# Kernel tuning notes

Hardware: AMD Instinct MI355X
Metric: run time of the kernel (lower is better)

## Reference

```python
import jax, jax.numpy as jnp
import numpy as np

DIM = 512
HIDDEN = int(DIM * 0.2)  # 102
K_TOKENS = 64
N_TOKENS = 65536
LN_EPS = 1e-5


def setup_inputs() -> dict:
    key = jax.random.key(0)
    ks = jax.random.split(key, 8)
    x = jax.random.normal(ks[0], (N_TOKENS, DIM), dtype=jnp.float32)
    ln_gamma = jnp.ones((DIM,), dtype=jnp.float32)
    ln_beta = jnp.zeros((DIM,), dtype=jnp.float32)
    W1 = jax.random.normal(ks[1], (DIM, HIDDEN), dtype=jnp.float32) / np.sqrt(DIM)
    b1 = jnp.zeros((HIDDEN,), dtype=jnp.float32)
    W2 = jax.random.normal(ks[2], (HIDDEN, K_TOKENS), dtype=jnp.float32) / np.sqrt(HIDDEN)
    b2 = jnp.zeros((K_TOKENS,), dtype=jnp.float32)
    scale = jnp.ones((1, 1), dtype=jnp.float32)
    return {
        "x": x,
        "ln_gamma": ln_gamma,
        "ln_beta": ln_beta,
        "W1": W1,
        "b1": b1,
        "W2": W2,
        "b2": b2,
        "scale": scale,
        "keeped_tokens": K_TOKENS,
    }


def reference(x, ln_gamma, ln_beta, W1, b1, W2, b2, scale, keeped_tokens):
    # LayerNorm over last dim
    mu = jnp.mean(x, axis=-1, keepdims=True)
    var = jnp.mean(jnp.square(x - mu), axis=-1, keepdims=True)
    h = (x - mu) * jax.lax.rsqrt(var + LN_EPS) * ln_gamma + ln_beta
    # fc1 + exact GELU (torch default) + dynamic fc2 scorer
    h = jax.nn.gelu(h @ W1 + b1, approximate=False)  # [N, HIDDEN]
    w = h @ W2 + b2                                   # [N, K]
    # transpose, scale, softmax over tokens
    w = w.T * scale                                   # [K, N]
    w = jax.nn.softmax(w, axis=1)
    # weighted token aggregation
    return w @ x                                      # [K, DIM]
```

## Files before the change

### kernel.cpp

```cpp
#include <hip/hip_runtime.h>
#include <math.h>

#define N_TOK 65536
#define DIM   512
#define HID   102
#define KTOK  64
#define NTILE 4096
#define LN_EPS 1e-5f

typedef __attribute__((ext_vector_type(8))) short short8;
typedef __attribute__((ext_vector_type(4))) float f32x4;

#define WS_LOGITS 0u
#define WS_PART   4194304u
#define WS_PM     (WS_PART + 4194304u)
#define WS_PS     (WS_PM + 262144u)
#define WS_W1F    (WS_PS + 262144u)
#define WS_W2F    (WS_W1F + 32768u)
#define WS_UB     (WS_W2F + 4096u)
#define WS_VV     (WS_UB + 128u)
#define WS_SMAX   (WS_VV + 128u)
#define WS_SINV   (WS_SMAX + 64u)

__device__ __forceinline__ unsigned short f2bf(float f) {
    unsigned int u = __float_as_uint(f);
    unsigned int r = (u + 0x7fffu + ((u >> 16) & 1u)) >> 16;
    return (unsigned short)r;
}
__device__ __forceinline__ float bf2f(unsigned short h) {
    return __uint_as_float(((unsigned int)h) << 16);
}

__device__ __forceinline__ void gload_lds16(const void* g, void* l) {
    __builtin_amdgcn_global_load_lds(
        (const __attribute__((address_space(1))) unsigned int*)g,
        (__attribute__((address_space(3))) unsigned int*)l, 16, 0, 0);
}

__device__ __forceinline__ void bar_lds() {
    asm volatile("s_waitcnt lgkmcnt(0)" ::: "memory");
    __builtin_amdgcn_s_barrier();
    __builtin_amdgcn_sched_barrier(0);
}

__global__ __launch_bounds__(256) void prep_k(const float* __restrict__ W1,
                                              const float* __restrict__ gamma,
                                              const float* __restrict__ W2,
                                              unsigned short* __restrict__ W1f,
                                              unsigned short* __restrict__ W2f) {
    const int idx = blockIdx.x * 256 + threadIdx.x;
    {
        const int e = idx & 7, lane = (idx >> 3) & 63;
        const int jj = (idx >> 9) & 7, kc = (idx >> 12) & 15;
        const int j = jj * 16 + (lane & 15);
        const int d = kc * 32 + (lane >> 4) * 8 + e;
        W1f[idx] = (j < HID) ? f2bf(gamma[d] * W1[d * HID + j]) : (unsigned short)0;
    }
    if (idx < 8192) {
        const int e = idx & 7, lane = (idx >> 3) & 63;
        const int kc = (idx >> 9) & 3, N = (idx >> 11) & 3;
        const int j = kc * 32 + (lane >> 4) * 8 + e;
        const int k = N * 16 + (lane & 15);
        W2f[idx] = (j < HID) ? f2bf(W2[j * KTOK + k]) : (unsigned short)0;
    }
}

__global__ __launch_bounds__(512) void prep2_k(const float* __restrict__ W1,
                                               const float* __restrict__ b1,
                                               const float* __restrict__ gamma,
                                               const float* __restrict__ beta,
                                               float* __restrict__ ub,
                                               float* __restrict__ vv) {
    __shared__ float su[4][128], sv[4][128];
    const int t = threadIdx.x;
    const int j = t & 127, q = t >> 7;
    float u = 0.0f, v = 0.0f;
    if (j < HID) {
        #pragma unroll 8
        for (int d = q * 128; d < q * 128 + 128; ++d) {
            const float wv = W1[d * HID + j];
            u = fmaf(beta[d], wv, u);
            v = fmaf(gamma[d], wv, v);
        }
    }
    su[q][j] = u; sv[q][j] = v;
    __syncthreads();
    if (q == 0) {
        ub[j] = su[0][j] + su[1][j] + su[2][j] + su[3][j] +
                ((j < HID) ? b1[j] : 0.0f);
        vv[j] = sv[0][j] + sv[1][j] + sv[2][j] + sv[3][j];
    }
}

__global__ __launch_bounds__(512) void scorer_k(const float* __restrict__ x,
                                                const unsigned short* __restrict__ W1f,
                                                const unsigned short* __restrict__ W2f,
                                                const float* __restrict__ ub,
                                                const float* __restrict__ vv,
                                                const float* __restrict__ b2,
                                                const float* __restrict__ scale,
                                                float* __restrict__ logits,
                                                float* __restrict__ pm,
                                                float* __restrict__ psum) {
    __shared__ char smem[4 * 8192];
    const int tid = threadIdx.x;
    const int lane = tid & 63;
    const int w = tid >> 6;
    const int l15 = lane & 15;
    const int hi = lane >> 4;
    const int tile = blockIdx.x * 8 + w;
    const int wt0 = tile * 16;
    char* hb = smem + w * 4096;

    gload_lds16(W1f + w * 512 + lane * 8, smem + w * 1024);
    gload_lds16(W1f + 4096 + w * 512 + lane * 8, smem + 8192 + w * 1024);

    const float* xrow = x + (size_t)(wt0 + l15) * DIM + hi * 8;
    float s = 0.0f, ss = 0.0f;
    #pragma unroll
    for (int kc = 0; kc < 16; ++kc) {
        const f32x4 a = *(const f32x4*)(xrow + kc * 32);
        const f32x4 b = *(const f32x4*)(xrow + kc * 32 + 4);
        s += a.x + a.y + a.z + a.w + b.x + b.y + b.z + b.w;
        ss += a.x * a.x + a.y * a.y + a.z * a.z + a.w * a.w +
              b.x * b.x + b.y * b.y + b.z * b.z + b.w * b.w;
        if ((kc & 7) == 7) __builtin_amdgcn_sched_barrier(0);
    }
    s += __shfl_xor(s, 16); ss += __shfl_xor(ss, 16);
    s += __shfl_xor(s, 32); ss += __shfl_xor(ss, 32);
    const float mu = s * (1.0f / 512.0f);
    const float inv = rsqrtf(ss * (1.0f / 512.0f) - mu * mu + LN_EPS);

    asm volatile("" : "+v"(xrow));

    f32x4 acc[8] = {};
    f32x4 xa = *(const f32x4*)(xrow);
    f32x4 xb = *(const f32x4*)(xrow + 4);
    #pragma unroll
    for (int kc = 0; kc < 16; ++kc) {
        f32x4 xa_n, xb_n;
        if (kc < 15) {
            xa_n = *(const f32x4*)(xrow + (kc + 1) * 32);
            xb_n = *(const f32x4*)(xrow + (kc + 1) * 32 + 4);
        }
        if (kc < 14) {
            gload_lds16(W1f + (kc + 2) * 4096 + w * 512 + lane * 8,
                        smem + ((kc + 2) & 3) * 8192 + w * 1024);
        }
        if (kc == 0 || kc == 14)
            asm volatile("s_waitcnt vmcnt(3)" ::: "memory");
        else if (kc < 14)
            asm volatile("s_waitcnt vmcnt(4)" ::: "memory");
        else
            asm volatile("s_waitcnt vmcnt(0)" ::: "memory");
        __builtin_amdgcn_sched_barrier(0);
        __builtin_amdgcn_s_barrier();
        short8 af;
        af[0] = (short)f2bf(xa.x); af[1] = (short)f2bf(xa.y);
        af[2] = (short)f2bf(xa.z); af[3] = (short)f2bf(xa.w);
        af[4] = (short)f2bf(xb.x); af[5] = (short)f2bf(xb.y);
        af[6] = (short)f2bf(xb.z); af[7] = (short)f2bf(xb.w);
        const char* bb = smem + (kc & 3) * 8192 + lane * 16;
        __builtin_amdgcn_s_setprio(1);
        #pragma unroll
        for (int jj = 0; jj < 8; ++jj) {
            const short8 bf = *(const short8*)(bb + jj * 1024);
            acc[jj] = __builtin_amdgcn_mfma_f32_16x16x32_bf16(af, bf, acc[jj], 0, 0, 0);
        }
        __builtin_amdgcn_s_setprio(0);
        xa = xa_n; xb = xb_n;
    }
    __syncthreads();

    float invr[4], muir[4];
    #pragma unroll
    for (int r = 0; r < 4; ++r) {
        const int tk = 4 * hi + r;
        const float m_ = __shfl(mu, tk);
        const float i_ = __shfl(inv, tk);
        invr[r] = i_;
        muir[r] = m_ * i_;
    }
    #pragma unroll
    for (int jj = 0; jj < 8; ++jj) {
        const int col = jj * 16 + l15;
        const float ubj = ub[col];
        const float vvj = vv[col];
        #pragma unroll
        for (int reg = 0; reg < 4; ++reg) {
            const int t = 4 * hi + reg;
            const float pre = fmaf(invr[reg], acc[jj][reg],
                                   fmaf(-muir[reg], vvj, ubj));
            const float g = 0.5f * pre * (1.0f + erff(pre * 0.70710678118f));
            *(unsigned short*)(hb + t * 256 + ((col * 2) ^ ((t & 7) << 4))) = f2bf(g);
        }
    }
    asm volatile("s_waitcnt lgkmcnt(0)" ::: "memory");
    __builtin_amdgcn_sched_barrier(0);

    f32x4 acc2[4] = {};
    {
        const unsigned short* w2 = W2f + lane * 8;
        #pragma unroll
        for (int kc = 0; kc < 4; ++kc) {
            const short8 a2 = *(const short8*)(hb + l15 * 256 +
                                               ((kc * 64 + hi * 16) ^ ((l15 & 7) << 4)));
            __builtin_amdgcn_s_setprio(1);
            #pragma unroll
            for (int nt = 0; nt < 4; ++nt) {
                const short8 bfr = *(const short8*)(w2 + (size_t)(nt * 4 + kc) * 512);
                acc2[nt] = __builtin_amdgcn_mfma_f32_16x16x32_bf16(a2, bfr, acc2[nt], 0, 0, 0);
            }
            __builtin_amdgcn_s_setprio(0);
        }
    }

    const float sc = scale[0];
    #pragma unroll
    for (int nt = 0; nt < 4; ++nt) {
        const int k = nt * 16 + l15;
        const float bb = b2[k];
        f32x4 lv;
        lv.x = (acc2[nt][0] + bb) * sc;
        lv.y = (acc2[nt][1] + bb) * sc;
        lv.z = (acc2[nt][2] + bb) * sc;
        lv.w = (acc2[nt][3] + bb) * sc;
        *(f32x4*)(logits + (size_t)k * N_TOK + wt0 + hi * 4) = lv;
        float m4 = fmaxf(fmaxf(lv.x, lv.y), fmaxf(lv.z, lv.w));
        float s4 = __expf(lv.x - m4) + __expf(lv.y - m4) +
                   __expf(lv.z - m4) + __expf(lv.w - m4);
        #pragma unroll
        for (int o = 16; o <= 32; o <<= 1) {
            const float om = __shfl_xor(m4, o);
            const float os = __shfl_xor(s4, o);
            const float nm = fmaxf(m4, om);
            s4 = s4 * __expf(m4 - nm) + os * __expf(om - nm);
            m4 = nm;
        }
        if (hi == 0) {
            pm[tile * 64 + k] = m4;
            psum[tile * 64 + k] = s4;
        }
    }
}

__global__ __launch_bounds__(256) void stats_k(const float* __restrict__ pm,
                                               const float* __restrict__ psum,
                                               float* __restrict__ smax,
                                               float* __restrict__ sinv) {
    const int k = blockIdx.x;
    const int tid = threadIdx.x;
    __shared__ float rm[4], rs[4];
    float m = -1e30f, s = 0.0f;
    for (int b = tid; b < NTILE; b += 256) {
        const float pmv = pm[b * 64 + k];
        const float psv = psum[b * 64 + k];
        const float nm = fmaxf(m, pmv);
        s = s * __expf(m - nm) + psv * __expf(pmv - nm);
        m = nm;
    }
    #pragma unroll
    for (int o = 32; o >= 1; o >>= 1) {
        const float om = __shfl_xor(m, o);
        const float os = __shfl_xor(s, o);
        const float nm = fmaxf(m, om);
        s = s * __expf(m - nm) + os * __expf(om - nm);
        m = nm;
    }
    if ((tid & 63) == 0) { rm[tid >> 6] = m; rs[tid >> 6] = s; }
    __syncthreads();
    if (tid == 0) {
        float fm = rm[0], fs = rs[0];
        for (int i = 1; i < 4; ++i) {
            const float nm = fmaxf(fm, rm[i]);
            fs = fs * __expf(fm - nm) + rs[i] * __expf(rm[i] - nm);
            fm = nm;
        }
        smax[k] = fm;
        sinv[k] = 1.0f / fs;
    }
}

__global__ __launch_bounds__(512) void agg_k(const float* __restrict__ x,
                                             const float* __restrict__ logits,
                                             const float* __restrict__ smax,
                                             const float* __restrict__ sinv,
                                             float* __restrict__ part) {
    __shared__ char fsm[40960];
    const int tid = threadIdx.x;
    const int lane = tid & 63;
    const int w = tid >> 6;
    const int l15 = lane & 15;
    const int hi = lane >> 4;
    const int dg = blockIdx.y;
    const int tb = blockIdx.x;

    const int sk = tid >> 3;
    const int snp = (tid & 7) * 8;
    const int xd = tid & 127;
    const int xnb = (tid >> 7) * 16;
    const float mk = smax[sk];
    const float ik = sinv[sk];
    const float* lrow = logits + (size_t)sk * N_TOK + tb * 512 + snp;
    const float* xcol = x + (size_t)(tb * 512 + xnb) * DIM + dg * 128 + xd;

    char* pw = fsm + (((sk >> 4) * 2 + (snp >> 5)) * 64 +
                      (sk & 15) + 16 * ((snp & 31) >> 3)) * 16;
    const int xoff0 = (((xd >> 4) * 2 + (xnb >> 5)) * 64 +
                       (xd & 15) + 16 * (((xnb & 31) >> 3) + 0)) * 16;
    const int xoff1 = (((xd >> 4) * 2 + (xnb >> 5)) * 64 +
                       (xd & 15) + 16 * (((xnb & 31) >> 3) + 1)) * 16;

    const int kt = w & 3;
    const int dgr = w >> 2;

    f32x4 acc[4] = {};

    f32x4 pa = *(const f32x4*)(lrow);
    f32x4 pb = *(const f32x4*)(lrow + 4);
    float xl[16];
    #pragma unroll
    for (int i = 0; i < 16; ++i) xl[i] = xcol[(size_t)i * DIM];

    for (int c = 0; c < 8; ++c) {
        {
            short8 pv;
            pv[0] = (short)f2bf(__expf(pa.x - mk) * ik);
            pv[1] = (short)f2bf(__expf(pa.y - mk) * ik);
            pv[2] = (short)f2bf(__expf(pa.z - mk) * ik);
            pv[3] = (short)f2bf(__expf(pa.w - mk) * ik);
            pv[4] = (short)f2bf(__expf(pb.x - mk) * ik);
            pv[5] = (short)f2bf(__expf(pb.y - mk) * ik);
            pv[6] = (short)f2bf(__expf(pb.z - mk) * ik);
            pv[7] = (short)f2bf(__expf(pb.w - mk) * ik);
            *(short8*)pw = pv;
        }
        {
            short8 h0, l0, h1, l1;
            #pragma unroll
            for (int e = 0; e < 8; ++e) {
                const float v = xl[e];
                const unsigned short hb16 = f2bf(v);
                h0[e] = (short)hb16;
                l0[e] = (short)f2bf(v - bf2f(hb16));
            }
            #pragma unroll
            for (int e = 0; e < 8; ++e) {
                const float v = xl[8 + e];
                const unsigned short hb16 = f2bf(v);
                h1[e] = (short)hb16;
                l1[e] = (short)f2bf(v - bf2f(hb16));
            }
            *(short8*)(fsm + 8192 + xoff0) = h0;
            *(short8*)(fsm + 24576 + xoff0) = l0;
            *(short8*)(fsm + 8192 + xoff1) = h1;
            *(short8*)(fsm + 24576 + xoff1) = l1;
        }
        f32x4 pa_n, pb_n;
        float xln[16];
        if (c < 7) {
            pa_n = *(const f32x4*)(lrow + (c + 1) * 64);
            pb_n = *(const f32x4*)(lrow + (c + 1) * 64 + 4);
            #pragma unroll
            for (int i = 0; i < 16; ++i)
                xln[i] = xcol[(size_t)((c + 1) * 64 + i) * DIM];
        }
        bar_lds();

        __builtin_amdgcn_s_setprio(1);
        #pragma unroll
        for (int ns = 0; ns < 2; ++ns) {
            const short8 af =
                *(const short8*)(fsm + ((kt * 2 + ns) * 64 + lane) * 16);
            #pragma unroll
            for (int dt = 0; dt < 4; ++dt) {
                const int dti = dgr * 4 + dt;
                const short8 bh = *(const short8*)(fsm + 8192 +
                                                   ((dti * 2 + ns) * 64 + lane) * 16);
                const short8 bl = *(const short8*)(fsm + 24576 +
                                                   ((dti * 2 + ns) * 64 + lane) * 16);
                acc[dt] = __builtin_amdgcn_mfma_f32_16x16x32_bf16(af, bh, acc[dt], 0, 0, 0);
                acc[dt] = __builtin_amdgcn_mfma_f32_16x16x32_bf16(af, bl, acc[dt], 0, 0, 0);
            }
        }
        __builtin_amdgcn_s_setprio(0);
        bar_lds();

        pa = pa_n; pb = pb_n;
        #pragma unroll
        for (int i = 0; i < 16; ++i) xl[i] = xln[i];
    }

    #pragma unroll
    for (int dt = 0; dt < 4; ++dt) {
        const int dcol = dg * 128 + (dgr * 4 + dt) * 16 + l15;
        #pragma unroll
        for (int reg = 0; reg < 4; ++reg) {
            const int k = kt * 16 + 4 * hi + reg;
            part[((size_t)tb * 64 + k) * 512 + dcol] = acc[dt][reg];
        }
    }
}

__global__ __launch_bounds__(256) void reduce_k(const float* __restrict__ part,
                                                float* __restrict__ out) {
    const int idx = blockIdx.x * 256 + threadIdx.x;
    const int k = idx >> 9, d = idx & 511;
    float s = 0.0f;
    for (int tb = 0; tb < 128; ++tb) s += part[((size_t)tb * 64 + k) * 512 + d];
    out[idx] = s;
}

extern "C" void kernel_launch(void* const* d_in, const int* in_sizes, int n_in,
                              void* d_out, int out_size, void* d_ws, size_t ws_size,
                              hipStream_t stream) {
    const float* x     = (const float*)d_in[0];
    const float* gamma = (const float*)d_in[1];
    const float* beta  = (const float*)d_in[2];
    const float* W1    = (const float*)d_in[3];
    const float* b1    = (const float*)d_in[4];
    const float* W2    = (const float*)d_in[5];
    const float* b2    = (const float*)d_in[6];
    const float* scale = (const float*)d_in[7];
    float* out = (float*)d_out;
    float* ws  = (float*)d_ws;

    float* logits = ws + WS_LOGITS;
    float* part   = ws + WS_PART;
    float* pm     = ws + WS_PM;
    float* psum   = ws + WS_PS;
    unsigned short* W1f = (unsigned short*)(ws + WS_W1F);
    unsigned short* W2f = (unsigned short*)(ws + WS_W2F);
    float* ubv  = ws + WS_UB;
    float* vvv  = ws + WS_VV;
    float* smax = ws + WS_SMAX;
    float* sinv = ws + WS_SINV;

    hipLaunchKernelGGL(prep_k, dim3(256), dim3(256), 0, stream,
                       W1, gamma, W2, W1f, W2f);
    hipLaunchKernelGGL(prep2_k, dim3(1), dim3(512), 0, stream,
                       W1, b1, gamma, beta, ubv, vvv);
    hipLaunchKernelGGL(scorer_k, dim3(NTILE / 8), dim3(512), 0, stream,
                       x, W1f, W2f, ubv, vvv, b2, scale, logits, pm, psum);
    hipLaunchKernelGGL(stats_k, dim3(KTOK), dim3(256), 0, stream,
                       pm, psum, smax, sinv);
    hipLaunchKernelGGL(agg_k, dim3(128, 4), dim3(512), 0, stream,
                       x, logits, smax, sinv, part);
    hipLaunchKernelGGL(reduce_k, dim3(128), dim3(256), 0, stream,
                       part, out);
}
```

Before: 116.1 us.

## Fuse LayerNorm statistics pass into fc1 MFMA loop to read x once

Merges the separate mean/variance pass over each token row into the fc1 matmul loop, so every x chunk is loaded once and used both for the statistics and for the bf16 MFMA operand. The x prefetch is deepened to a three-slot register ring, and the vmcnt waits are retuned for the interleaved x and W1 loads. This drops the second global read of x (the dominant traffic) at the cost of more live registers and a tighter wait schedule, and it relies on LN being applied after the matmul through the mu/inv correction already present.

```diff
diff --git a/kernel.cpp b/kernel.cpp
--- a/kernel.cpp
+++ b/kernel.cpp
@@ -112,65 +112,59 @@
     const int wt0 = tile * 16;
     char* hb = smem + w * 4096;
 
+    const float* xrow = x + (size_t)(wt0 + l15) * DIM + hi * 8;
+
+    f32x4 xva[3], xvb[3];
+    xva[0] = *(const f32x4*)(xrow);
+    xvb[0] = *(const f32x4*)(xrow + 4);
     gload_lds16(W1f + w * 512 + lane * 8, smem + w * 1024);
+    xva[1] = *(const f32x4*)(xrow + 32);
+    xvb[1] = *(const f32x4*)(xrow + 36);
     gload_lds16(W1f + 4096 + w * 512 + lane * 8, smem + 8192 + w * 1024);
 
-    const float* xrow = x + (size_t)(wt0 + l15) * DIM + hi * 8;
+    f32x4 acc[8] = {};
     float s = 0.0f, ss = 0.0f;
     #pragma unroll
     for (int kc = 0; kc < 16; ++kc) {
-        const f32x4 a = *(const f32x4*)(xrow + kc * 32);
-        const f32x4 b = *(const f32x4*)(xrow + kc * 32 + 4);
+        if (kc < 14) {
+            xva[(kc + 2) % 3] = *(const f32x4*)(xrow + (kc + 2) * 32);
+            xvb[(kc + 2) % 3] = *(const f32x4*)(xrow + (kc + 2) * 32 + 4);
+            gload_lds16(W1f + (kc + 2) * 4096 + w * 512 + lane * 8,
+                        smem + ((kc + 2) & 3) * 8192 + w * 1024);
+        }
+        if (kc < 14)
+            asm volatile("s_waitcnt vmcnt(6)" ::: "memory");
+        else if (kc == 14)
+            asm volatile("s_waitcnt vmcnt(3)" ::: "memory");
+        else
+            asm volatile("s_waitcnt vmcnt(0)" ::: "memory");
+        __builtin_amdgcn_sched_barrier(0);
+        __builtin_amdgcn_s_barrier();
+        const f32x4 a = xva[kc % 3];
+        const f32x4 b = xvb[kc % 3];
         s += a.x + a.y + a.z + a.w + b.x + b.y + b.z + b.w;
         ss += a.x * a.x + a.y * a.y + a.z * a.z + a.w * a.w +
               b.x * b.x + b.y * b.y + b.z * b.z + b.w * b.w;
-        if ((kc & 7) == 7) __builtin_amdgcn_sched_barrier(0);
-    }
+        short8 af;
+        af[0] = (short)f2bf(a.x); af[1] = (short)f2bf(a.y);
+        af[2] = (short)f2bf(a.z); af[3] = (short)f2bf(a.w);
+        af[4] = (short)f2bf(b.x); af[5] = (short)f2bf(b.y);
+        af[6] = (short)f2bf(b.z); af[7] = (short)f2bf(b.w);
+        const char* bb = smem + (kc & 3) * 8192 + lane * 16;
+        __builtin_amdgcn_s_setprio(1);
+        #pragma unroll
+        for (int jj = 0; jj < 8; ++jj) {
+            const short8 bf = *(const short8*)(bb + jj * 1024);
+            acc[jj] = __builtin_amdgcn_mfma_f32_16x16x32_bf16(af, bf, acc[jj], 0, 0, 0);
+        }
+        __builtin_amdgcn_s_setprio(0);
+    }
+    __syncthreads();
+
     s += __shfl_xor(s, 16); ss += __shfl_xor(ss, 16);
     s += __shfl_xor(s, 32); ss += __shfl_xor(ss, 32);
     const float mu = s * (1.0f / 512.0f);
     const float inv = rsqrtf(ss * (1.0f / 512.0f) - mu * mu + LN_EPS);
-
-    asm volatile("" : "+v"(xrow));
-
-    f32x4 acc[8] = {};
-    f32x4 xa = *(const f32x4*)(xrow);
-    f32x4 xb = *(const f32x4*)(xrow + 4);
-    #pragma unroll
-    for (int kc = 0; kc < 16; ++kc) {
-        f32x4 xa_n, xb_n;
-        if (kc < 15) {
-            xa_n = *(const f32x4*)(xrow + (kc + 1) * 32);
-            xb_n = *(const f32x4*)(xrow + (kc + 1) * 32 + 4);
-        }
-        if (kc < 14) {
-            gload_lds16(W1f + (kc + 2) * 4096 + w * 512 + lane * 8,
-                        smem + ((kc + 2) & 3) * 8192 + w * 1024);
-        }
-        if (kc == 0 || kc == 14)
-            asm volatile("s_waitcnt vmcnt(3)" ::: "memory");
-        else if (kc < 14)
-            asm volatile("s_waitcnt vmcnt(4)" ::: "memory");
-        else
-            asm volatile("s_waitcnt vmcnt(0)" ::: "memory");
-        __builtin_amdgcn_sched_barrier(0);
-        __builtin_amdgcn_s_barrier();
-        short8 af;
-        af[0] = (short)f2bf(xa.x); af[1] = (short)f2bf(xa.y);
-        af[2] = (short)f2bf(xa.z); af[3] = (short)f2bf(xa.w);
-        af[4] = (short)f2bf(xb.x); af[5] = (short)f2bf(xb.y);
-        af[6] = (short)f2bf(xb.z); af[7] = (short)f2bf(xb.w);
-        const char* bb = smem + (kc & 3) * 8192 + lane * 16;
-        __builtin_amdgcn_s_setprio(1);
-        #pragma unroll
-        for (int jj = 0; jj < 8; ++jj) {
-            const short8 bf = *(const short8*)(bb + jj * 1024);
-            acc[jj] = __builtin_amdgcn_mfma_f32_16x16x32_bf16(af, bf, acc[jj], 0, 0, 0);
-        }
-        __builtin_amdgcn_s_setprio(0);
-        xa = xa_n; xb = xb_n;
-    }
-    __syncthreads();
 
     float invr[4], muir[4];
     #pragma unroll
```

Measured after the change: 108.0 us. 6.9% less time.
